# Performance work log

Measured on AMD Instinct MI355X. Metric: run time of the kernel, lower is better.

## Reference

```python
import jax, jax.numpy as jnp
import numpy as np

N, D = 1048576, 64

def setup_inputs() -> dict:
    key = jax.random.key(0)
    k1, k2, k3 = jax.random.split(key, 3)
    S2_out = jax.random.normal(k1, (N, D), dtype=jnp.float32)
    A1_out = jax.random.normal(k2, (N, D), dtype=jnp.float32)
    labels = jax.random.randint(k3, (N,), 0, 3, dtype=jnp.int64)
    return {"S2_out": S2_out, "A1_out": A1_out, "labels": labels}

def reference(S2_out, A1_out, labels):
    # row-wise L2 distance between A1_out and S2_out (torch.dist(a, b, 2) per row)
    diff = A1_out - S2_out
    d = jnp.sqrt(jnp.sum(diff * diff, axis=-1))  # [N]
    t = jnp.tanh(d)
    # label == 2 -> relu(1 - tanh(d)); otherwise -> relu(1 + tanh(d))
    sign = jnp.where(labels == 2, -1.0, 1.0).astype(S2_out.dtype)
    err = jax.nn.relu(1.0 + sign * t)
    return jnp.sum(err)
```

## Files before the change

kernel.cpp:

```cpp
#include <hip/hip_runtime.h>
#include <hip/hip_bf16.h>


#define BLOCK 256
#define GRID  2048

__global__ __launch_bounds__(BLOCK) void loss_antonymy_kernel(
    const float4* __restrict__ S2,
    const float4* __restrict__ A1,
    const int*    __restrict__ labels,
    float* __restrict__ out,
    int n_rows)
{
    const int tid      = blockIdx.x * BLOCK + threadIdx.x;
    const int group    = tid >> 4;
    const int lane16   = threadIdx.x & 15;
    const int n_groups = (GRID * BLOCK) >> 4;

    float acc = 0.0f;

    for (int row = group; row < n_rows; row += n_groups) {
        const int base = (row << 4) + lane16;
        float4 a = A1[base];
        float4 s = S2[base];
        float dx = a.x - s.x;
        float dy = a.y - s.y;
        float dz = a.z - s.z;
        float dw = a.w - s.w;
        float ss = dx*dx + dy*dy + dz*dz + dw*dw;

        ss += __shfl_xor(ss, 1, 16);
        ss += __shfl_xor(ss, 2, 16);
        ss += __shfl_xor(ss, 4, 16);
        ss += __shfl_xor(ss, 8, 16);

        if (lane16 == 0) {
            float d = sqrtf(ss);
            float t = tanhf(d);
            float sign = (labels[row] == 2) ? -1.0f : 1.0f;
            acc += fmaxf(1.0f + sign * t, 0.0f);
        }
    }

    for (int off = 32; off > 0; off >>= 1)
        acc += __shfl_down(acc, off, 64);

    __shared__ float wsum[BLOCK / 64];
    const int wave = threadIdx.x >> 6;
    const int lane = threadIdx.x & 63;
    if (lane == 0) wsum[wave] = acc;
    __syncthreads();

    if (wave == 0) {
        float v = (lane < (BLOCK / 64)) ? wsum[lane] : 0.0f;
        for (int off = 2; off > 0; off >>= 1)
            v += __shfl_down(v, off, 64);
        if (lane == 0) atomicAdd(out, v);
    }
}

extern "C" void kernel_launch(void* const* d_in, const int* in_sizes, int n_in,
                              void* d_out, int out_size, void* d_ws, size_t ws_size,
                              hipStream_t stream) {
    const float4* S2     = (const float4*)d_in[0];
    const float4* A1     = (const float4*)d_in[1];
    const int*    labels = (const int*)d_in[2];
    float* out = (float*)d_out;

    const int n_rows = in_sizes[2];

    hipMemsetAsync(out, 0, sizeof(float), stream);

    loss_antonymy_kernel<<<GRID, BLOCK, 0, stream>>>(S2, A1, labels, out, n_rows);
}
```

Measured before the change: 510.2 us.

## Map four threads per row with two rows per iteration and fast tanh

Rows are now handled by groups of 4 threads instead of 16. Each thread loads four float4 values per array, and each iteration processes two rows, which raises the number of loads in flight per thread and cuts shuffle work. tanhf is replaced with an exp/reciprocal formulation that uses hardware intrinsics, which slightly changes precision. Register pressure rises, which could reduce occupancy.

```diff
diff --git a/kernel.cpp b/kernel.cpp
--- a/kernel.cpp
+++ b/kernel.cpp
@@ -4,6 +4,41 @@
 
 #define BLOCK 256
 #define GRID  2048
+
+__device__ __forceinline__ float fast_err(float ss, int lab) {
+    float d = sqrtf(ss);
+    float e = __expf(2.0f * d);
+    float t = 1.0f - 2.0f * __builtin_amdgcn_rcpf(e + 1.0f);
+    float sgn = (lab == 2) ? -1.0f : 1.0f;
+    return fmaxf(fmaf(sgn, t, 1.0f), 0.0f);
+}
+
+__device__ __forceinline__ float row_ss(const float4* __restrict__ A,
+                                        const float4* __restrict__ S,
+                                        int row, int l4) {
+    const float4* pa = A + (row << 4) + l4;
+    const float4* ps = S + (row << 4) + l4;
+    float4 a0 = pa[0], a1 = pa[4], a2 = pa[8], a3 = pa[12];
+    float4 s0 = ps[0], s1 = ps[4], s2 = ps[8], s3 = ps[12];
+    float p0, p1, p2, p3, dx;
+    dx = a0.x - s0.x; p0 = dx * dx;
+    dx = a0.y - s0.y; p0 = fmaf(dx, dx, p0);
+    dx = a0.z - s0.z; p0 = fmaf(dx, dx, p0);
+    dx = a0.w - s0.w; p0 = fmaf(dx, dx, p0);
+    dx = a1.x - s1.x; p1 = dx * dx;
+    dx = a1.y - s1.y; p1 = fmaf(dx, dx, p1);
+    dx = a1.z - s1.z; p1 = fmaf(dx, dx, p1);
+    dx = a1.w - s1.w; p1 = fmaf(dx, dx, p1);
+    dx = a2.x - s2.x; p2 = dx * dx;
+    dx = a2.y - s2.y; p2 = fmaf(dx, dx, p2);
+    dx = a2.z - s2.z; p2 = fmaf(dx, dx, p2);
+    dx = a2.w - s2.w; p2 = fmaf(dx, dx, p2);
+    dx = a3.x - s3.x; p3 = dx * dx;
+    dx = a3.y - s3.y; p3 = fmaf(dx, dx, p3);
+    dx = a3.z - s3.z; p3 = fmaf(dx, dx, p3);
+    dx = a3.w - s3.w; p3 = fmaf(dx, dx, p3);
+    return (p0 + p1) + (p2 + p3);
+}
 
 __global__ __launch_bounds__(BLOCK) void loss_antonymy_kernel(
     const float4* __restrict__ S2,
@@ -13,33 +48,32 @@
     int n_rows)
 {
     const int tid      = blockIdx.x * BLOCK + threadIdx.x;
-    const int group    = tid >> 4;
-    const int lane16   = threadIdx.x & 15;
-    const int n_groups = (GRID * BLOCK) >> 4;
+    const int group    = tid >> 2;
+    const int l4       = threadIdx.x & 3;
+    const int n_groups = (GRID * BLOCK) >> 2;
 
     float acc = 0.0f;
 
-    for (int row = group; row < n_rows; row += n_groups) {
-        const int base = (row << 4) + lane16;
-        float4 a = A1[base];
-        float4 s = S2[base];
-        float dx = a.x - s.x;
-        float dy = a.y - s.y;
-        float dz = a.z - s.z;
-        float dw = a.w - s.w;
-        float ss = dx*dx + dy*dy + dz*dz + dw*dw;
+    for (int row = group; row < n_rows; row += 2 * n_groups) {
+        const int rowA = row;
+        const int rowB = row + n_groups;
+        const bool hasB = (rowB < n_rows);
 
-        ss += __shfl_xor(ss, 1, 16);
-        ss += __shfl_xor(ss, 2, 16);
-        ss += __shfl_xor(ss, 4, 16);
-        ss += __shfl_xor(ss, 8, 16);
+        int labA = labels[rowA];
+        int labB = hasB ? labels[rowB] : 0;
 
-        if (lane16 == 0) {
-            float d = sqrtf(ss);
-            float t = tanhf(d);
-            float sign = (labels[row] == 2) ? -1.0f : 1.0f;
-            acc += fmaxf(1.0f + sign * t, 0.0f);
-        }
+        float ssA = row_ss(A1, S2, rowA, l4);
+        float ssB = hasB ? row_ss(A1, S2, rowB, l4) : 0.0f;
+
+        ssA += __shfl_xor(ssA, 1, 4);
+        ssB += __shfl_xor(ssB, 1, 4);
+        ssA += __shfl_xor(ssA, 2, 4);
+        ssB += __shfl_xor(ssB, 2, 4);
+
+        float errA = fast_err(ssA, labA);
+        float errB = hasB ? fast_err(ssB, labB) : 0.0f;
+
+        if (l4 == 0) acc += errA + errB;
     }
 
     for (int off = 32; off > 0; off >>= 1)
```

Result: no change. 504.4 us (-1.1%).
